# Kernel optimization log

Measured on AMD Instinct MI355X. Metric: run time of the kernel, lower is better.

Reference implementation:

```python
import jax, jax.numpy as jnp
import numpy as np

B, S, D, T = 64, 512, 768, 64


def setup_inputs() -> dict:
    key = jax.random.key(0)
    k1, k2, k3 = jax.random.split(key, 3)
    x = jax.random.normal(k1, (B, S, D), dtype=jnp.float32)
    W = jax.random.normal(k2, (T, D), dtype=jnp.float32) * 0.02
    b = jnp.zeros((T,), dtype=jnp.float32)
    transitions = jax.random.uniform(k3, (T, T), dtype=jnp.float32, minval=-0.1, maxval=0.1)
    return {"x": x, "W": W, "b": b, "transitions": transitions}


def reference(x, W, b, transitions):
    # emissions: [B,S,T] -> [S,B,T]
    em = jnp.einsum('bsd,td->bst', x, W) + b
    em = em.transpose(1, 0, 2)

    # Viterbi forward: max-plus scan over time, collecting argmax backpointers
    def step(score, em_t):
        # score: [B,T] (prev tag), em_t: [B,T] (cur tag)
        s = score[:, :, None] + transitions[None, :, :] + em_t[:, None, :]  # [B,Tprev,Tcur]
        return jnp.max(s, axis=1), jnp.argmax(s, axis=1)

    final_score, history = jax.lax.scan(step, em[0], em[1:])  # history: [S-1,B,T]

    # Backtrack (vectorized over batch) with a reverse scan
    best = jnp.argmax(final_score, axis=-1)  # [B]

    def back(nxt, idx_t):
        prev = jnp.take_along_axis(idx_t, nxt[:, None], axis=1)[:, 0]  # [B]
        return prev, prev

    _, prev_tags = jax.lax.scan(back, best, history, reverse=True)  # [S-1,B], tags for t=0..S-2
    tags = jnp.concatenate([prev_tags, best[None, :]], axis=0)  # [S,B]
    return tags.T.astype(jnp.int32)  # [B,S]
```

## Files before the change

### kernel.cpp

```cpp
#include <hip/hip_runtime.h>

#define SS 512
#define DD 768
#define TT 64

typedef __attribute__((ext_vector_type(2))) float f32x2;

__device__ __forceinline__ f32x2 vmax2(f32x2 a, f32x2 b) {
    return __builtin_elementwise_max(a, b);
}

__global__ __launch_bounds__(256) void emis_gemm(
    const float* __restrict__ X, const float* __restrict__ W,
    const float* __restrict__ bias, float* __restrict__ em)
{
    __shared__ __align__(16) float Xs[16][68];
    __shared__ __align__(16) float Ws[16][68];

    const int tid = threadIdx.x;
    const int m0  = blockIdx.x * 64;
    const int tm  = tid >> 4;
    const int tn  = tid & 15;
    const int lr  = tid >> 2;
    const int lk  = tid & 3;

    float acc[4][4];
#pragma unroll
    for (int i = 0; i < 4; i++)
#pragma unroll
        for (int j = 0; j < 4; j++) acc[i][j] = 0.f;

    float4 xr, wr;
    xr = *(const float4*)&X[(size_t)(m0 + lr) * DD + lk * 4];
    wr = *(const float4*)&W[(size_t)lr * DD + lk * 4];

    for (int t = 0; t < 48; t++) {
        Xs[lk * 4 + 0][lr] = xr.x;  Xs[lk * 4 + 1][lr] = xr.y;
        Xs[lk * 4 + 2][lr] = xr.z;  Xs[lk * 4 + 3][lr] = xr.w;
        Ws[lk * 4 + 0][lr] = wr.x;  Ws[lk * 4 + 1][lr] = wr.y;
        Ws[lk * 4 + 2][lr] = wr.z;  Ws[lk * 4 + 3][lr] = wr.w;
        __syncthreads();

        if (t < 47) {
            const int k0 = (t + 1) * 16;
            xr = *(const float4*)&X[(size_t)(m0 + lr) * DD + k0 + lk * 4];
            wr = *(const float4*)&W[(size_t)lr * DD + k0 + lk * 4];
        }

#pragma unroll
        for (int k = 0; k < 16; k++) {
            float a[4], bv[4];
            *(float4*)&a[0]  = *(const float4*)&Xs[k][tm * 4];
            *(float4*)&bv[0] = *(const float4*)&Ws[k][tn * 4];
#pragma unroll
            for (int i = 0; i < 4; i++)
#pragma unroll
                for (int j = 0; j < 4; j++)
                    acc[i][j] = fmaf(a[i], bv[j], acc[i][j]);
        }
        __syncthreads();
    }

    const float4 bv4 = *(const float4*)&bias[tn * 4];
#pragma unroll
    for (int i = 0; i < 4; i++) {
        const size_t row = (size_t)(m0 + tm * 4 + i);
        float4 o;
        o.x = acc[i][0] + bv4.x;  o.y = acc[i][1] + bv4.y;
        o.z = acc[i][2] + bv4.z;  o.w = acc[i][3] + bv4.w;
        *(float4*)&em[row * TT + tn * 4] = o;
    }
}

__global__ __launch_bounds__(64)
__attribute__((amdgpu_waves_per_eu(1, 1)))
void viterbi_fwd(
    const float* __restrict__ em, const float* __restrict__ trans,
    float* __restrict__ scoreHist, int* __restrict__ bestTag)
{
    __shared__ __align__(16) float sc_lds[TT];
    __shared__ __align__(16) float tr_lds[4096];

    const int b    = blockIdx.x;
    const int lane = threadIdx.x;
    const float* emb = em + (size_t)b * SS * TT;
    float* sh = scoreHist + (size_t)b * SS * TT;

    {
        float4* dst = (float4*)tr_lds;
        const float4* src = (const float4*)trans;
#pragma unroll
        for (int i = 0; i < 16; i++) dst[lane + i * 64] = src[lane + i * 64];
    }
    __syncthreads();

    f32x2 tpk[32];
#pragma unroll
    for (int j = 0; j < 32; j++) {
        tpk[j].x = tr_lds[(2 * j) * TT + lane];
        tpk[j].y = tr_lds[(2 * j + 1) * TT + lane];
    }

    const float em0 = emb[lane];
    sc_lds[lane] = em0;
    sh[lane] = em0;
    float sc = em0;

    float er0 = emb[1 * TT + lane];
    float er1 = emb[2 * TT + lane];
    float er2 = emb[3 * TT + lane];
    float er3 = emb[4 * TT + lane];

    float4 sq[16];
    {
        const float4* sb = (const float4*)sc_lds;
#pragma unroll
        for (int i = 0; i < 16; i++) sq[i] = sb[i];
    }

    auto step = [&](int s, float em_v) {
        const f32x2* sq2 = (const f32x2*)sq;
        f32x2 pk[32];
#pragma unroll
        for (int j = 0; j < 32; j++) pk[j] = sq2[j] + tpk[j];

#pragma unroll
        for (int m = 16; m >= 1; m >>= 1)
#pragma unroll
            for (int j = 0; j < 16; j++) {
                if (j < m) pk[j] = vmax2(pk[j], pk[j + m]);
            }
        sc = fmaxf(pk[0].x, pk[0].y) + em_v;

        sc_lds[lane] = sc;
        {
            const float4* sb = (const float4*)sc_lds;
#pragma unroll
            for (int i = 0; i < 16; i++) sq[i] = sb[i];
        }
        sh[s * TT + lane] = sc;
    };

    for (int sb = 1; sb <= 505; sb += 4) {
        step(sb + 0, er0);  er0 = emb[(sb + 4) * TT + lane];
        step(sb + 1, er1);  er1 = emb[(sb + 5) * TT + lane];
        step(sb + 2, er2);  er2 = emb[(sb + 6) * TT + lane];
        step(sb + 3, er3);  er3 = emb[((sb + 7) <= 511 ? (sb + 7) : 511) * TT + lane];
    }
    step(509, er0);
    step(510, er1);
    step(511, er2);

    float fv = sc;
    int   fa = lane;
#pragma unroll
    for (int m = 1; m <= 32; m <<= 1) {
        const float vo = __shfl_xor(fv, m, 64);
        const int   ao = __shfl_xor(fa, m, 64);
        if (vo > fv || (vo == fv && ao < fa)) { fv = vo; fa = ao; }
    }
    if (lane == 0) bestTag[b] = fa;
}

__global__ __launch_bounds__(256) void bp_kernel(
    const float* __restrict__ scoreHist, const float* __restrict__ em,
    const float* __restrict__ trans, unsigned char* __restrict__ hist8)
{
    __shared__ __align__(16) float tr_lds[4096];
    const int tid = threadIdx.x;
    {
        const float4* src = (const float4*)trans;
        float4* dst = (float4*)tr_lds;
        for (int i = tid; i < 1024; i += 256) dst[i] = src[i];
    }
    __syncthreads();

    const int wv   = tid >> 6;
    const int lane = tid & 63;
    const int g    = blockIdx.x * 4 + wv;
    const int b    = g / 511;
    const int s    = 1 + (g % 511);

    const float4* sb4 = (const float4*)(scoreHist + ((size_t)b * SS + (s - 1)) * TT);
    const float em_v = em[((size_t)b * SS + s) * TT + lane];

    float treg[TT];
#pragma unroll
    for (int p = 0; p < TT; p++) treg[p] = tr_lds[p * TT + lane];

    float4 sq[16];
#pragma unroll
    for (int i = 0; i < 16; i++) sq[i] = sb4[i];

    float v[TT];
#pragma unroll
    for (int i = 0; i < 16; i++) {
        v[4 * i + 0] = (sq[i].x + treg[4 * i + 0]) + em_v;
        v[4 * i + 1] = (sq[i].y + treg[4 * i + 1]) + em_v;
        v[4 * i + 2] = (sq[i].z + treg[4 * i + 2]) + em_v;
        v[4 * i + 3] = (sq[i].w + treg[4 * i + 3]) + em_v;
    }
    float m1[32]; int a1[32];
#pragma unroll
    for (int i = 0; i < 32; i++) {
        const bool t = v[2 * i + 1] > v[2 * i];
        m1[i] = t ? v[2 * i + 1] : v[2 * i];
        a1[i] = 2 * i + (t ? 1 : 0);
    }
    float m2[16]; int a2[16];
#pragma unroll
    for (int i = 0; i < 16; i++) {
        const bool t = m1[2 * i + 1] > m1[2 * i];
        m2[i] = t ? m1[2 * i + 1] : m1[2 * i];
        a2[i] = t ? a1[2 * i + 1] : a1[2 * i];
    }
    float m3[8]; int a3[8];
#pragma unroll
    for (int i = 0; i < 8; i++) {
        const bool t = m2[2 * i + 1] > m2[2 * i];
        m3[i] = t ? m2[2 * i + 1] : m2[2 * i];
        a3[i] = t ? a2[2 * i + 1] : a2[2 * i];
    }
    float m4[4]; int a4[4];
#pragma unroll
    for (int i = 0; i < 4; i++) {
        const bool t = m3[2 * i + 1] > m3[2 * i];
        m4[i] = t ? m3[2 * i + 1] : m3[2 * i];
        a4[i] = t ? a3[2 * i + 1] : a3[2 * i];
    }
    float m5[2]; int a5[2];
#pragma unroll
    for (int i = 0; i < 2; i++) {
        const bool t = m4[2 * i + 1] > m4[2 * i];
        m5[i] = t ? m4[2 * i + 1] : m4[2 * i];
        a5[i] = t ? a4[2 * i + 1] : a4[2 * i];
    }
    const bool t6 = m5[1] > m5[0];
    const int barg = t6 ? a5[1] : a5[0];

    hist8[((size_t)b * SS + s) * TT + lane] = (unsigned char)barg;
}

__global__ __launch_bounds__(1024) void backtrack(
    const unsigned char* __restrict__ hist8, const int* __restrict__ bestTag,
    int* __restrict__ out)
{
    __shared__ unsigned char A[511 * 64];
    __shared__ unsigned char Bf[511 * 64];

    const int b   = blockIdx.x;
    const int tid = threadIdx.x;
    const unsigned char* h8 = hist8 + (size_t)b * SS * TT;

    for (int idx = tid; idx < 511 * 64; idx += 1024) A[idx] = h8[idx + 64];
    __syncthreads();

    unsigned char* curT = A;
    unsigned char* nxtT = Bf;
    for (int d = 1; d < 511; d <<= 1) {
        for (int gQ = 0; gQ < 7; gQ++) {
            int i0 = tid + (gQ * 4 + 0) * 1024;
            int i1 = tid + (gQ * 4 + 1) * 1024;
            int i2 = tid + (gQ * 4 + 2) * 1024;
            int i3 = tid + (gQ * 4 + 3) * 1024;
            int s0 = i0 >> 6, s1 = i1 >> 6, s2 = i2 >> 6, s3 = i3 >> 6;
            int a0 = (s0 + d >= 511) ? i0 : (s0 + d) * 64 + (i0 & 63);
            int a1 = (s1 + d >= 511) ? i1 : (s1 + d) * 64 + (i1 & 63);
            int a2 = (s2 + d >= 511) ? i2 : (s2 + d) * 64 + (i2 & 63);
            int a3 = (s3 + d >= 511) ? i3 : (s3 + d) * 64 + (i3 & 63);
            unsigned char q0 = curT[a0], q1 = curT[a1], q2 = curT[a2], q3 = curT[a3];
            int f0 = (s0 + d >= 511) ? i0 : s0 * 64 + q0;
            int f1 = (s1 + d >= 511) ? i1 : s1 * 64 + q1;
            int f2 = (s2 + d >= 511) ? i2 : s2 * 64 + q2;
            int f3 = (s3 + d >= 511) ? i3 : s3 * 64 + q3;
            nxtT[i0] = curT[f0];  nxtT[i1] = curT[f1];
            nxtT[i2] = curT[f2];  nxtT[i3] = curT[f3];
        }
        for (int j = 28; j < 31; j++) {
            int i0 = tid + j * 1024;
            int s0 = i0 >> 6;
            int a0 = (s0 + d >= 511) ? i0 : (s0 + d) * 64 + (i0 & 63);
            unsigned char q0 = curT[a0];
            int f0 = (s0 + d >= 511) ? i0 : s0 * 64 + q0;
            nxtT[i0] = curT[f0];
        }
        {
            int i0 = tid + 31 * 1024;
            if (i0 < 511 * 64) {
                int s0 = i0 >> 6;
                int a0 = (s0 + d >= 511) ? i0 : (s0 + d) * 64 + (i0 & 63);
                unsigned char q0 = curT[a0];
                int f0 = (s0 + d >= 511) ? i0 : s0 * 64 + q0;
                nxtT[i0] = curT[f0];
            }
        }
        __syncthreads();
        unsigned char* tmp = curT; curT = nxtT; nxtT = tmp;
    }

    const int bt = bestTag[b];
    for (int s = tid; s < SS; s += 1024) {
        const int tag = (s == 511) ? bt : (int)curT[s * 64 + bt];
        out[(size_t)b * SS + s] = tag;
    }
}

extern "C" void kernel_launch(void* const* d_in, const int* in_sizes, int n_in,
                              void* d_out, int out_size, void* d_ws, size_t ws_size,
                              hipStream_t stream)
{
    const float* X     = (const float*)d_in[0];
    const float* W     = (const float*)d_in[1];
    const float* bias  = (const float*)d_in[2];
    const float* trans = (const float*)d_in[3];
    int* out = (int*)d_out;

    char* ws = (char*)d_ws;
    float*         em        = (float*)ws;
    float*         scoreHist = (float*)(ws + 8388608);
    unsigned char* hist8     = (unsigned char*)(ws + 16777216);
    int*           bestTag   = (int*)(ws + 18874368);

    emis_gemm<<<dim3(512), dim3(256), 0, stream>>>(X, W, bias, em);
    viterbi_fwd<<<dim3(64), dim3(64), 0, stream>>>(em, trans, scoreHist, bestTag);
    bp_kernel<<<dim3(8176), dim3(256), 0, stream>>>(scoreHist, em, trans, hist8);
    backtrack<<<dim3(64), dim3(1024), 0, stream>>>(hist8, bestTag, out);
}
```

Baseline: 267.9 us.

## Recover argmax by equality with stored score; backtrack serially with readlane

The backpointer kernel no longer runs a 64-way max/argmax tree. It finds the first predecessor whose recomputed score equals the already stored forward score, which relies on both passes computing bitwise-identical values. The backtrack kernel swaps the pointer-jumping doubling scheme over LDS, which used 1024 threads per batch, for a single wavefront. That wavefront follows the chain sequentially with readlane and prefetches history rows four steps ahead. This trades parallel log-depth work for a 511-step serial dependency chain with low per-step latency.

Result: faster. 227.4 us (-15.1%).

```diff
diff --git a/kernel.cpp b/kernel.cpp
--- a/kernel.cpp
+++ b/kernel.cpp
@@ -181,128 +181,82 @@
     const int b    = g / 511;
     const int s    = 1 + (g % 511);
 
-    const float4* sb4 = (const float4*)(scoreHist + ((size_t)b * SS + (s - 1)) * TT);
+    const f32x2* sb2 = (const f32x2*)(scoreHist + ((size_t)b * SS + (s - 1)) * TT);
     const float em_v = em[((size_t)b * SS + s) * TT + lane];
-
-    float treg[TT];
-#pragma unroll
-    for (int p = 0; p < TT; p++) treg[p] = tr_lds[p * TT + lane];
-
-    float4 sq[16];
-#pragma unroll
-    for (int i = 0; i < 16; i++) sq[i] = sb4[i];
-
-    float v[TT];
-#pragma unroll
-    for (int i = 0; i < 16; i++) {
-        v[4 * i + 0] = (sq[i].x + treg[4 * i + 0]) + em_v;
-        v[4 * i + 1] = (sq[i].y + treg[4 * i + 1]) + em_v;
-        v[4 * i + 2] = (sq[i].z + treg[4 * i + 2]) + em_v;
-        v[4 * i + 3] = (sq[i].w + treg[4 * i + 3]) + em_v;
-    }
-    float m1[32]; int a1[32];
-#pragma unroll
-    for (int i = 0; i < 32; i++) {
-        const bool t = v[2 * i + 1] > v[2 * i];
-        m1[i] = t ? v[2 * i + 1] : v[2 * i];
-        a1[i] = 2 * i + (t ? 1 : 0);
-    }
-    float m2[16]; int a2[16];
-#pragma unroll
-    for (int i = 0; i < 16; i++) {
-        const bool t = m1[2 * i + 1] > m1[2 * i];
-        m2[i] = t ? m1[2 * i + 1] : m1[2 * i];
-        a2[i] = t ? a1[2 * i + 1] : a1[2 * i];
-    }
-    float m3[8]; int a3[8];
-#pragma unroll
-    for (int i = 0; i < 8; i++) {
-        const bool t = m2[2 * i + 1] > m2[2 * i];
-        m3[i] = t ? m2[2 * i + 1] : m2[2 * i];
-        a3[i] = t ? a2[2 * i + 1] : a2[2 * i];
-    }
-    float m4[4]; int a4[4];
-#pragma unroll
-    for (int i = 0; i < 4; i++) {
-        const bool t = m3[2 * i + 1] > m3[2 * i];
-        m4[i] = t ? m3[2 * i + 1] : m3[2 * i];
-        a4[i] = t ? a3[2 * i + 1] : a3[2 * i];
-    }
-    float m5[2]; int a5[2];
-#pragma unroll
-    for (int i = 0; i < 2; i++) {
-        const bool t = m4[2 * i + 1] > m4[2 * i];
-        m5[i] = t ? m4[2 * i + 1] : m4[2 * i];
-        a5[i] = t ? a4[2 * i + 1] : a4[2 * i];
-    }
-    const bool t6 = m5[1] > m5[0];
-    const int barg = t6 ? a5[1] : a5[0];
-
-    hist8[((size_t)b * SS + s) * TT + lane] = (unsigned char)barg;
-}
-
-__global__ __launch_bounds__(1024) void backtrack(
+    const float sh_v = scoreHist[((size_t)b * SS + s) * TT + lane];
+
+    f32x2 tpk[32];
+#pragma unroll
+    for (int j = 0; j < 32; j++) {
+        tpk[j].x = tr_lds[(2 * j) * TT + lane];
+        tpk[j].y = tr_lds[(2 * j + 1) * TT + lane];
+    }
+
+    f32x2 em2; em2.x = em_v; em2.y = em_v;
+    f32x2 v2[32];
+#pragma unroll
+    for (int j = 0; j < 32; j++) {
+        f32x2 cand = sb2[j] + tpk[j];
+        v2[j] = cand + em2;
+    }
+
+    int idx = 63;
+#pragma unroll
+    for (int j = 31; j >= 0; j--) {
+        idx = (v2[j].y == sh_v) ? 2 * j + 1 : idx;
+        idx = (v2[j].x == sh_v) ? 2 * j     : idx;
+    }
+
+    hist8[((size_t)b * SS + s) * TT + lane] = (unsigned char)idx;
+}
+
+__global__ __launch_bounds__(64) void backtrack(
     const unsigned char* __restrict__ hist8, const int* __restrict__ bestTag,
     int* __restrict__ out)
 {
-    __shared__ unsigned char A[511 * 64];
-    __shared__ unsigned char Bf[511 * 64];
-
-    const int b   = blockIdx.x;
-    const int tid = threadIdx.x;
+    __shared__ int tags[SS];
+
+    const int b    = blockIdx.x;
+    const int lane = threadIdx.x;
     const unsigned char* h8 = hist8 + (size_t)b * SS * TT;
 
-    for (int idx = tid; idx < 511 * 64; idx += 1024) A[idx] = h8[idx + 64];
+    int tag = bestTag[b];
+    if (lane == 0) tags[511] = tag;
+
+    int r0 = h8[511 * TT + lane];
+    int r1 = h8[510 * TT + lane];
+    int r2 = h8[509 * TT + lane];
+    int r3 = h8[508 * TT + lane];
+
+    for (int sb = 511; sb >= 11; sb -= 4) {
+        tag = __builtin_amdgcn_readlane(r0, tag);
+        if (lane == 0) tags[sb - 1] = tag;
+        r0 = h8[(sb - 4) * TT + lane];
+        tag = __builtin_amdgcn_readlane(r1, tag);
+        if (lane == 0) tags[sb - 2] = tag;
+        r1 = h8[(sb - 5) * TT + lane];
+        tag = __builtin_amdgcn_readlane(r2, tag);
+        if (lane == 0) tags[sb - 3] = tag;
+        r2 = h8[(sb - 6) * TT + lane];
+        tag = __builtin_amdgcn_readlane(r3, tag);
+        if (lane == 0) tags[sb - 4] = tag;
+        r3 = h8[(sb - 7) * TT + lane];
+    }
+    tag = __builtin_amdgcn_readlane(r0, tag);  if (lane == 0) tags[6] = tag;
+    tag = __builtin_amdgcn_readlane(r1, tag);  if (lane == 0) tags[5] = tag;
+    tag = __builtin_amdgcn_readlane(r2, tag);  if (lane == 0) tags[4] = tag;
+    tag = __builtin_amdgcn_readlane(r3, tag);  if (lane == 0) tags[3] = tag;
+    int q0 = h8[3 * TT + lane];
+    int q1 = h8[2 * TT + lane];
+    int q2 = h8[1 * TT + lane];
+    tag = __builtin_amdgcn_readlane(q0, tag);  if (lane == 0) tags[2] = tag;
+    tag = __builtin_amdgcn_readlane(q1, tag);  if (lane == 0) tags[1] = tag;
+    tag = __builtin_amdgcn_readlane(q2, tag);  if (lane == 0) tags[0] = tag;
+
     __syncthreads();
-
-    unsigned char* curT = A;
-    unsigned char* nxtT = Bf;
-    for (int d = 1; d < 511; d <<= 1) {
-        for (int gQ = 0; gQ < 7; gQ++) {
-            int i0 = tid + (gQ * 4 + 0) * 1024;
-            int i1 = tid + (gQ * 4 + 1) * 1024;
-            int i2 = tid + (gQ * 4 + 2) * 1024;
-            int i3 = tid + (gQ * 4 + 3) * 1024;
-            int s0 = i0 >> 6, s1 = i1 >> 6, s2 = i2 >> 6, s3 = i3 >> 6;
-            int a0 = (s0 + d >= 511) ? i0 : (s0 + d) * 64 + (i0 & 63);
-            int a1 = (s1 + d >= 511) ? i1 : (s1 + d) * 64 + (i1 & 63);
-            int a2 = (s2 + d >= 511) ? i2 : (s2 + d) * 64 + (i2 & 63);
-            int a3 = (s3 + d >= 511) ? i3 : (s3 + d) * 64 + (i3 & 63);
-            unsigned char q0 = curT[a0], q1 = curT[a1], q2 = curT[a2], q3 = curT[a3];
-            int f0 = (s0 + d >= 511) ? i0 : s0 * 64 + q0;
-            int f1 = (s1 + d >= 511) ? i1 : s1 * 64 + q1;
-            int f2 = (s2 + d >= 511) ? i2 : s2 * 64 + q2;
-            int f3 = (s3 + d >= 511) ? i3 : s3 * 64 + q3;
-            nxtT[i0] = curT[f0];  nxtT[i1] = curT[f1];
-            nxtT[i2] = curT[f2];  nxtT[i3] = curT[f3];
-        }
-        for (int j = 28; j < 31; j++) {
-            int i0 = tid + j * 1024;
-            int s0 = i0 >> 6;
-            int a0 = (s0 + d >= 511) ? i0 : (s0 + d) * 64 + (i0 & 63);
-            unsigned char q0 = curT[a0];
-            int f0 = (s0 + d >= 511) ? i0 : s0 * 64 + q0;
-            nxtT[i0] = curT[f0];
-        }
-        {
-            int i0 = tid + 31 * 1024;
-            if (i0 < 511 * 64) {
-                int s0 = i0 >> 6;
-                int a0 = (s0 + d >= 511) ? i0 : (s0 + d) * 64 + (i0 & 63);
-                unsigned char q0 = curT[a0];
-                int f0 = (s0 + d >= 511) ? i0 : s0 * 64 + q0;
-                nxtT[i0] = curT[f0];
-            }
-        }
-        __syncthreads();
-        unsigned char* tmp = curT; curT = nxtT; nxtT = tmp;
-    }
-
-    const int bt = bestTag[b];
-    for (int s = tid; s < SS; s += 1024) {
-        const int tag = (s == 511) ? bt : (int)curT[s * 64 + bt];
-        out[(size_t)b * SS + s] = tag;
-    }
+#pragma unroll
+    for (int s = 0; s < 8; s++)
+        out[(size_t)b * SS + s * 64 + lane] = tags[s * 64 + lane];
 }
 
 extern "C" void kernel_launch(void* const* d_in, const int* in_sizes, int n_in,
@@ -324,5 +278,5 @@
     emis_gemm<<<dim3(512), dim3(256), 0, stream>>>(X, W, bias, em);
     viterbi_fwd<<<dim3(64), dim3(64), 0, stream>>>(em, trans, scoreHist, bestTag);
     bp_kernel<<<dim3(8176), dim3(256), 0, stream>>>(scoreHist, em, trans, hist8);
-    backtrack<<<dim3(64), dim3(1024), 0, stream>>>(hist8, bestTag, out);
-}
+    backtrack<<<dim3(64), dim3(64), 0, stream>>>(hist8, bestTag, out);
+}
```
